# Performance work log

Hardware: AMD Instinct MI355X
Metric: run time of the kernel (lower is better)

## Reference

```python
import jax, jax.numpy as jnp
import numpy as np
from jax import lax

B, L, C = 128, 200, 300          # batch, text_len, embed_channels
K = 128                          # conv_num_kernel
WS = (2, 3, 4, 5)                # conv_kernel_size
A = 5000                         # num_api
F = 64                           # feature_channels


def setup_inputs() -> dict:
    key = jax.random.key(0)
    ks = jax.random.split(key, 24)
    s = 0.02
    inp = {"x": jax.random.normal(ks[0], (B, L, C), dtype=jnp.float32)}
    for i, ws in enumerate(WS):
        inp[f"conv_w{ws}"] = jax.random.normal(ks[1 + i], (K, C, ws), dtype=jnp.float32) * s
        inp[f"conv_b{ws}"] = jnp.zeros((K,), dtype=jnp.float32)
    D = K * len(WS)
    inp["sc_fcl_w"] = jax.random.normal(ks[5], (A, D), dtype=jnp.float32) * s
    inp["sc_fcl_b"] = jnp.zeros((A,), dtype=jnp.float32)
    inp["fic_fc_w"] = jax.random.normal(ks[6], (F, D), dtype=jnp.float32) * s
    inp["fic_fc_b"] = jnp.zeros((F,), dtype=jnp.float32)
    inp["emb"] = jax.random.uniform(ks[7], (F, A), dtype=jnp.float32)  # torch.rand
    inp["mlp_w1"] = jax.random.normal(ks[8], (F, 2 * F), dtype=jnp.float32) * s
    inp["mlp_b1"] = jnp.zeros((F,), dtype=jnp.float32)
    inp["mlp_w2"] = jax.random.normal(ks[9], (1, F), dtype=jnp.float32) * s
    inp["mlp_b2"] = jnp.zeros((1,), dtype=jnp.float32)
    inp["fic_fcl_w"] = jax.random.normal(ks[10], (A, 2 * A), dtype=jnp.float32) * s
    inp["fic_fcl_b"] = jnp.zeros((A,), dtype=jnp.float32)
    inp["fusion_w"] = jax.random.normal(ks[11], (A, 2 * A), dtype=jnp.float32) * s
    inp["fusion_b"] = jnp.zeros((A,), dtype=jnp.float32)
    inp["task_w"] = jax.random.normal(ks[12], (A, A), dtype=jnp.float32) * s
    inp["task_b"] = jnp.zeros((A,), dtype=jnp.float32)
    return inp


def _textcnn(x_t, conv_ws, conv_bs):
    # x_t: (B, C, L); each branch: conv1d VALID -> relu -> global max over width -> (B, K)
    feats = []
    for w, b in zip(conv_ws, conv_bs):
        y = lax.conv_general_dilated(x_t, w, (1,), 'VALID',
                                     dimension_numbers=('NCH', 'OIH', 'NCH'))
        y = jax.nn.relu(y + b[None, :, None])
        feats.append(jnp.max(y, axis=2))  # full-width max-pool -> (B, K)
    # torch: cat along width dim=2 of (B,K,1) then view(B,-1) -> kernel-window index fastest
    return jnp.stack(feats, axis=2).reshape(x_t.shape[0], -1)  # (B, K*len(WS))


def reference(x, conv_w2, conv_b2, conv_w3, conv_b3, conv_w4, conv_b4,
              conv_w5, conv_b5, sc_fcl_w, sc_fcl_b, fic_fc_w, fic_fc_b, emb,
              mlp_w1, mlp_b1, mlp_w2, mlp_b2, fic_fcl_w, fic_fcl_b,
              fusion_w, fusion_b, task_w, task_b):
    x_t = jnp.transpose(x, (0, 2, 1))  # (B, C, L)
    e = _textcnn(x_t, (conv_w2, conv_w3, conv_w4, conv_w5),
                 (conv_b2, conv_b3, conv_b4, conv_b5))  # (B, D)

    u_sc = e @ sc_fcl_w.T + sc_fcl_b          # (B, A)
    u_sc_trans = e @ fic_fc_w.T + fic_fc_b    # (B, F)
    u_mm = u_sc_trans @ emb                   # (B, A)

    # Batched form of the per-sample repeat/concat + MLP loop:
    # concat(u_rep, emb.T) @ W1.T  ==  u @ W1[:, :F].T (bcast over A) + emb.T @ W1[:, F:].T
    h = (u_sc_trans @ mlp_w1[:, :F].T)[:, None, :] \
        + (emb.T @ mlp_w1[:, F:].T)[None, :, :] + mlp_b1  # (B, A, F)
    u_mlp = jnp.tanh(jnp.einsum('baf,f->ba', h, mlp_w2[0]) + mlp_b2[0])  # (B, A)

    u_fic = jnp.tanh(jnp.concatenate([u_mm, u_mlp], axis=1) @ fic_fcl_w.T + fic_fcl_b)
    u_mmf = jnp.concatenate([u_sc, u_fic], axis=1) @ fusion_w.T + fusion_b
    task = u_mmf @ task_w.T + task_b          # (B, A)
    return task
```

## Files before the change

### kernel.cpp

```cpp
#include <hip/hip_runtime.h>
#include <math.h>

#define B_ 128
#define L_ 200
#define C_ 300
#define K_ 128
#define A_ 5000
#define F_ 64
#define D_ 512
#define CP_ 320
#define LP_ 260
#define NPAD_ 5056
#define KP2_ 10048
#define KP1_ 5056

typedef __attribute__((ext_vector_type(8))) short bf16x8;
typedef __attribute__((ext_vector_type(8))) short short8;
typedef __attribute__((ext_vector_type(4))) float f32x4;

#define MFMA(a,b,c) __builtin_amdgcn_mfma_f32_16x16x32_bf16(a,b,c,0,0,0)

static __device__ __forceinline__ unsigned short f2bf(float f) {
    unsigned u = __float_as_uint(f);
    unsigned r = (u + 0x7FFFu + ((u >> 16) & 1u)) >> 16;
    return (unsigned short)r;
}

#define OFF_XP     ((size_t)0)
#define OFF_PART   ((size_t)0)
#define OFF_WP     ((size_t)5324800)
#define OFF_E      ((size_t)5611520)
#define OFF_EBF    ((size_t)5677056)
#define OFF_UMBF   ((size_t)5324800)
#define OFF_UMMFBF ((size_t)5324800)
#define OFF_UST    ((size_t)5967872)
#define OFF_VB     ((size_t)5976064)
#define OFF_S2     ((size_t)5976128)
#define OFF_T      ((size_t)5976256)
#define OFF_UFBF   ((size_t)5981312)

__global__ __launch_bounds__(320) void prep_x_kernel(const float* __restrict__ x, short* __restrict__ xp)
{
    const int row = blockIdx.x;
    const int b   = blockIdx.y;
    const int c   = threadIdx.x;
    float v = 0.f;
    if (row < L_ && c < C_) v = x[((size_t)b * L_ + row) * C_ + c];
    xp[((size_t)b * LP_ + row) * CP_ + c] = (short)f2bf(v);
}

__global__ void prep_w_kernel(const float* __restrict__ w2, const float* __restrict__ w3,
                              const float* __restrict__ w4, const float* __restrict__ w5,
                              short* __restrict__ wp)
{
    const int idx = blockIdx.x * 256 + threadIdx.x;
    if (idx >= 128 * 14 * CP_) return;
    int off, wsz; const float* src;
    if (idx < 81920)       { off = idx;          wsz = 2; src = w2; }
    else if (idx < 204800) { off = idx - 81920;  wsz = 3; src = w3; }
    else if (idx < 368640) { off = idx - 204800; wsz = 4; src = w4; }
    else                   { off = idx - 368640; wsz = 5; src = w5; }
    const int k   = off / (wsz * CP_);
    const int r   = off % (wsz * CP_);
    const int tap = r / CP_;
    const int c   = r % CP_;
    float v = 0.f;
    if (c < C_) v = src[((size_t)k * C_ + c) * wsz + tap];
    wp[idx] = (short)f2bf(v);
}

__global__ __launch_bounds__(512) void conv_gemm2_kernel(
    const short* __restrict__ xp, const short* __restrict__ wp,
    const float* __restrict__ b2, const float* __restrict__ b3,
    const float* __restrict__ b4, const float* __restrict__ b5,
    float* __restrict__ e)
{
    const int b  = blockIdx.x;
    const int br = blockIdx.y;
    const int nt = blockIdx.z;
    const int wsz  = br + 2;
    const int Pout = 199 - br;
    const int wbase = (br == 0) ? 0 : (br == 1) ? 81920 : (br == 2) ? 204800 : 368640;

    const int tid  = threadIdx.x;
    const int wave = tid >> 6;
    const int lane = tid & 63;
    const int mw   = wave & 3;
    const int nw   = wave >> 2;

    __shared__ short lA[260 * 36];
    __shared__ short lB[5 * 64 * 36];
    __shared__ float smax[4][64];

    f32x4 acc[4][2];
    #pragma unroll
    for (int mf = 0; mf < 4; ++mf)
        #pragma unroll
        for (int nf = 0; nf < 2; ++nf)
            acc[mf][nf] = (f32x4){0.f, 0.f, 0.f, 0.f};

    for (int cc = 0; cc < 10; ++cc) {
        for (int ch = tid; ch < 1040; ch += 512) {
            const int row = ch >> 2, half = ch & 3;
            *(short8*)(lA + row * 36 + half * 8) =
                *(const short8*)(xp + ((size_t)b * LP_ + row) * CP_ + cc * 32 + half * 8);
        }
        for (int ch = tid; ch < wsz * 256; ch += 512) {
            const int tap = ch >> 8;
            const int r2  = ch & 255;
            const int fil = r2 >> 2, half = r2 & 3;
            *(short8*)(lB + (tap * 64 + fil) * 36 + half * 8) =
                *(const short8*)(wp + wbase + (size_t)(nt * 64 + fil) * (wsz * CP_) + tap * CP_ + cc * 32 + half * 8);
        }
        __syncthreads();
        for (int tap = 0; tap < wsz; ++tap) {
            bf16x8 af[4], bfr[2];
            #pragma unroll
            for (int mf = 0; mf < 4; ++mf)
                af[mf] = *(const bf16x8*)(lA + (mw * 64 + mf * 16 + (lane & 15) + tap) * 36 + (lane >> 4) * 8);
            #pragma unroll
            for (int nf = 0; nf < 2; ++nf)
                bfr[nf] = *(const bf16x8*)(lB + (tap * 64 + nw * 32 + nf * 16 + (lane & 15)) * 36 + (lane >> 4) * 8);
            #pragma unroll
            for (int mf = 0; mf < 4; ++mf)
                #pragma unroll
                for (int nf = 0; nf < 2; ++nf)
                    acc[mf][nf] = MFMA(af[mf], bfr[nf], acc[mf][nf]);
        }
        __syncthreads();
    }

    float vm0 = -1e30f, vm1 = -1e30f;
    #pragma unroll
    for (int mf = 0; mf < 4; ++mf) {
        const int rowbase = mw * 64 + mf * 16 + (lane >> 4) * 4;
        #pragma unroll
        for (int r = 0; r < 4; ++r) {
            const bool valid = (rowbase + r) < Pout;
            vm0 = fmaxf(vm0, valid ? acc[mf][0][r] : -1e30f);
            vm1 = fmaxf(vm1, valid ? acc[mf][1][r] : -1e30f);
        }
    }
    vm0 = fmaxf(vm0, __shfl_xor(vm0, 16)); vm0 = fmaxf(vm0, __shfl_xor(vm0, 32));
    vm1 = fmaxf(vm1, __shfl_xor(vm1, 16)); vm1 = fmaxf(vm1, __shfl_xor(vm1, 32));
    if (lane < 16) {
        smax[mw][nw * 32 + lane]      = vm0;
        smax[mw][nw * 32 + 16 + lane] = vm1;
    }
    __syncthreads();
    if (tid < 64) {
        const float m = fmaxf(fmaxf(smax[0][tid], smax[1][tid]), fmaxf(smax[2][tid], smax[3][tid]));
        const int k = nt * 64 + tid;
        const float* bp = (br == 0) ? b2 : (br == 1) ? b3 : (br == 2) ? b4 : b5;
        e[(size_t)b * D_ + k * 4 + br] = fmaxf(bp[k] + m, 0.f);
    }
}

__global__ void prep_u_kernel(const float* __restrict__ src, int srcld,
                              short* __restrict__ dst, int ncols, int Kpad)
{
    const int idx = blockIdx.x * 256 + threadIdx.x;
    if (idx >= B_ * Kpad) return;
    const int b = idx / Kpad;
    const int c = idx % Kpad;
    float v = (c < ncols) ? src[(size_t)b * srcld + c] : 0.f;
    dst[idx] = (short)f2bf(v);
}

__global__ __launch_bounds__(512) void gemm2_kernel(
    const short* __restrict__ Abf, int Kpad,
    const float* __restrict__ W, int K, int N,
    int steps_per_z, float* __restrict__ partial)
{
    const int n0 = blockIdx.x * 64;
    const int total = Kpad >> 6;
    const int sbeg = blockIdx.y * steps_per_z;
    const int send = min(sbeg + steps_per_z, total);

    const int tid  = threadIdx.x;
    const int wave = tid >> 6;
    const int lane = tid & 63;
    const int mw   = wave & 3;
    const int nw   = wave >> 2;

    __shared__ short lA[128 * 68];
    __shared__ short lB[64 * 68];

    const int arow = tid >> 2, ac0 = (tid & 3) * 16;
    const int fil  = tid >> 3, wc0 = (tid & 7) * 8;

    f32x4 acc[2][2];
    #pragma unroll
    for (int mf = 0; mf < 2; ++mf)
        #pragma unroll
        for (int nf = 0; nf < 2; ++nf)
            acc[mf][nf] = (f32x4){0.f, 0.f, 0.f, 0.f};

    short8 ra0, ra1;
    float4 rw0, rw1;
    const bool wrow_ok = (n0 + fil) < N;

    {
        const int kb = sbeg * 64;
        ra0 = *(const short8*)(Abf + (size_t)arow * Kpad + kb + ac0);
        ra1 = *(const short8*)(Abf + (size_t)arow * Kpad + kb + ac0 + 8);
        rw0 = make_float4(0.f,0.f,0.f,0.f); rw1 = rw0;
        if (wrow_ok && (kb + wc0) < K)     rw0 = *(const float4*)(W + (size_t)(n0 + fil) * K + kb + wc0);
        if (wrow_ok && (kb + wc0 + 4) < K) rw1 = *(const float4*)(W + (size_t)(n0 + fil) * K + kb + wc0 + 4);
    }

    for (int s = sbeg; s < send; ++s) {
        __syncthreads();
        *(short8*)(lA + arow * 68 + ac0)     = ra0;
        *(short8*)(lA + arow * 68 + ac0 + 8) = ra1;
        {
            short8 wb;
            wb[0]=(short)f2bf(rw0.x); wb[1]=(short)f2bf(rw0.y); wb[2]=(short)f2bf(rw0.z); wb[3]=(short)f2bf(rw0.w);
            wb[4]=(short)f2bf(rw1.x); wb[5]=(short)f2bf(rw1.y); wb[6]=(short)f2bf(rw1.z); wb[7]=(short)f2bf(rw1.w);
            *(short8*)(lB + fil * 68 + wc0) = wb;
        }
        if (s + 1 < send) {
            const int kb = (s + 1) * 64;
            ra0 = *(const short8*)(Abf + (size_t)arow * Kpad + kb + ac0);
            ra1 = *(const short8*)(Abf + (size_t)arow * Kpad + kb + ac0 + 8);
            float4 t0 = make_float4(0.f,0.f,0.f,0.f), t1 = t0;
            if (wrow_ok && (kb + wc0) < K)     t0 = *(const float4*)(W + (size_t)(n0 + fil) * K + kb + wc0);
            if (wrow_ok && (kb + wc0 + 4) < K) t1 = *(const float4*)(W + (size_t)(n0 + fil) * K + kb + wc0 + 4);
            rw0 = t0; rw1 = t1;
        }
        __syncthreads();
        #pragma unroll
        for (int ks = 0; ks < 2; ++ks) {
            bf16x8 af[2], bfr[2];
            #pragma unroll
            for (int mf = 0; mf < 2; ++mf)
                af[mf] = *(const bf16x8*)(lA + (mw * 32 + mf * 16 + (lane & 15)) * 68 + ks * 32 + (lane >> 4) * 8);
            #pragma unroll
            for (int nf = 0; nf < 2; ++nf)
                bfr[nf] = *(const bf16x8*)(lB + (nw * 32 + nf * 16 + (lane & 15)) * 68 + ks * 32 + (lane >> 4) * 8);
            #pragma unroll
            for (int mf = 0; mf < 2; ++mf)
                #pragma unroll
                for (int nf = 0; nf < 2; ++nf)
                    acc[mf][nf] = MFMA(af[mf], bfr[nf], acc[mf][nf]);
        }
    }

    #pragma unroll
    for (int mf = 0; mf < 2; ++mf)
        #pragma unroll
        for (int nf = 0; nf < 2; ++nf)
            #pragma unroll
            for (int r = 0; r < 4; ++r) {
                const int row = mw * 32 + mf * 16 + (lane >> 4) * 4 + r;
                const int col = nw * 32 + nf * 16 + (lane & 15);
                partial[((size_t)blockIdx.y * B_ + row) * NPAD_ + n0 + col] = acc[mf][nf][r];
            }
}

__global__ void reduce2_kernel(const float* __restrict__ partial, const float* __restrict__ bias,
                               float* __restrict__ outf, short* __restrict__ outb,
                               int N, int ldo, int ooff, int js, int act)
{
    const int idx = blockIdx.x * 256 + threadIdx.x;
    if (idx >= B_ * N) return;
    const int n = idx % N;
    const int b = idx / N;
    float s = bias[n];
    for (int k = 0; k < js; ++k) s += partial[((size_t)k * B_ + b) * NPAD_ + n];
    if (act) s = tanhf(s);
    if (outb) outb[(size_t)b * ldo + ooff + n] = (short)f2bf(s);
    else      outf[(size_t)b * ldo + ooff + n] = s;
}

__global__ __launch_bounds__(256) void ust_kernel(
    const float* __restrict__ e, const float* __restrict__ W,
    const float* __restrict__ bias, float* __restrict__ ust)
{
    const int b = blockIdx.x;
    const int f = threadIdx.x >> 2;
    const int q = threadIdx.x & 3;
    const float* er = e + (size_t)b * D_ + q * 128;
    const float* wr = W + (size_t)f * D_ + q * 128;
    float acc = 0.f;
    #pragma unroll
    for (int j = 0; j < 128; j += 4) {
        const float4 ev = *(const float4*)(er + j);
        const float4 wv = *(const float4*)(wr + j);
        acc += ev.x*wv.x + ev.y*wv.y + ev.z*wv.z + ev.w*wv.w;
    }
    acc += __shfl_xor(acc, 1);
    acc += __shfl_xor(acc, 2);
    if (q == 0) ust[(size_t)b * F_ + f] = acc + bias[f];
}

__global__ void prep_kernel(const float* __restrict__ mlp_w1, const float* __restrict__ mlp_b1,
                            const float* __restrict__ mlp_w2, const float* __restrict__ mlp_b2,
                            const float* __restrict__ ust,
                            float* __restrict__ vB, float* __restrict__ s2)
{
    __shared__ float vA[64];
    __shared__ float csh;
    const int tid = threadIdx.x;
    if (tid < 64) {
        float a = 0.f;
        for (int f = 0; f < 64; ++f) a += mlp_w2[f] * mlp_w1[f * 128 + tid];
        vA[tid] = a;
    } else {
        const int g = tid - 64;
        float bsum = 0.f;
        for (int f = 0; f < 64; ++f) bsum += mlp_w2[f] * mlp_w1[f * 128 + 64 + g];
        vB[g] = bsum;
    }
    if (tid == 0) {
        float c = mlp_b2[0];
        for (int f = 0; f < 64; ++f) c += mlp_b1[f] * mlp_w2[f];
        csh = c;
    }
    __syncthreads();
    float s = csh;
    const float* ub = ust + (size_t)tid * F_;
    for (int g = 0; g < 64; ++g) s += ub[g] * vA[g];
    s2[tid] = s;
}

__global__ void ta_kernel(const float* __restrict__ emb, const float* __restrict__ vB,
                          float* __restrict__ t)
{
    __shared__ float v[64];
    if (threadIdx.x < 64) v[threadIdx.x] = vB[threadIdx.x];
    __syncthreads();
    const int a = blockIdx.x * 256 + threadIdx.x;
    if (a < A_) {
        float acc = 0.f;
        #pragma unroll
        for (int g = 0; g < 64; ++g) acc += v[g] * emb[(size_t)g * A_ + a];
        t[a] = acc;
    }
}

__global__ void um2_kernel(const float* __restrict__ ust, const float* __restrict__ emb,
                           const float* __restrict__ s2, const float* __restrict__ t,
                           short* __restrict__ umb)
{
    const int b = blockIdx.y;
    __shared__ float us[64];
    if (threadIdx.x < 64) us[threadIdx.x] = ust[(size_t)b * F_ + threadIdx.x];
    __syncthreads();
    const int a = blockIdx.x * 256 + threadIdx.x;
    if (a < A_) {
        float acc = 0.f;
        #pragma unroll
        for (int g = 0; g < 64; ++g) acc += us[g] * emb[(size_t)g * A_ + a];
        umb[(size_t)b * KP2_ + a] = (short)f2bf(acc);
        umb[(size_t)b * KP2_ + A_ + a] = (short)f2bf(tanhf(s2[b] + t[a]));
    } else if (a < A_ + 48) {
        umb[(size_t)b * KP2_ + A_ + a] = 0;
    }
}

__global__ void pad_kernel(short* __restrict__ buf, int ld, int c0, int n)
{
    const int b = blockIdx.x;
    for (int c = threadIdx.x; c < n; c += 64)
        buf[(size_t)b * ld + c0 + c] = 0;
}

extern "C" void kernel_launch(void* const* d_in, const int* in_sizes, int n_in,
                              void* d_out, int out_size, void* d_ws, size_t ws_size,
                              hipStream_t stream)
{
    const float* x       = (const float*)d_in[0];
    const float* conv_w2 = (const float*)d_in[1];
    const float* conv_b2 = (const float*)d_in[2];
    const float* conv_w3 = (const float*)d_in[3];
    const float* conv_b3 = (const float*)d_in[4];
    const float* conv_w4 = (const float*)d_in[5];
    const float* conv_b4 = (const float*)d_in[6];
    const float* conv_w5 = (const float*)d_in[7];
    const float* conv_b5 = (const float*)d_in[8];
    const float* sc_fcl_w = (const float*)d_in[9];
    const float* sc_fcl_b = (const float*)d_in[10];
    const float* fic_fc_w = (const float*)d_in[11];
    const float* fic_fc_b = (const float*)d_in[12];
    const float* emb      = (const float*)d_in[13];
    const float* mlp_w1   = (const float*)d_in[14];
    const float* mlp_b1   = (const float*)d_in[15];
    const float* mlp_w2   = (const float*)d_in[16];
    const float* mlp_b2   = (const float*)d_in[17];
    const float* fic_fcl_w = (const float*)d_in[18];
    const float* fic_fcl_b = (const float*)d_in[19];
    const float* fusion_w  = (const float*)d_in[20];
    const float* fusion_b  = (const float*)d_in[21];
    const float* task_w    = (const float*)d_in[22];
    const float* task_b    = (const float*)d_in[23];

    float* ws = (float*)d_ws;
    short* xp     = (short*)(ws + OFF_XP);
    float* part   = ws + OFF_PART;
    short* wp     = (short*)(ws + OFF_WP);
    float* e      = ws + OFF_E;
    short* ebf    = (short*)(ws + OFF_EBF);
    short* umbf   = (short*)(ws + OFF_UMBF);
    short* ummfbf = (short*)(ws + OFF_UMMFBF);
    float* ust    = ws + OFF_UST;
    float* vB     = ws + OFF_VB;
    float* s2     = ws + OFF_S2;
    float* t      = ws + OFF_T;
    short* ufbf   = (short*)(ws + OFF_UFBF);
    float* out    = (float*)d_out;

    prep_x_kernel<<<dim3(LP_, B_), CP_, 0, stream>>>(x, xp);
    prep_w_kernel<<<(128*14*CP_ + 255)/256, 256, 0, stream>>>(conv_w2, conv_w3, conv_w4, conv_w5, wp);

    conv_gemm2_kernel<<<dim3(B_, 4, 2), 512, 0, stream>>>(xp, wp, conv_b2, conv_b3, conv_b4, conv_b5, e);

    prep_u_kernel<<<(B_*D_ + 255)/256, 256, 0, stream>>>(e, D_, ebf, D_, D_);

    gemm2_kernel<<<dim3(79, 4), 512, 0, stream>>>(ebf, D_, sc_fcl_w, D_, A_, 2, part);
    reduce2_kernel<<<(B_*A_ + 255)/256, 256, 0, stream>>>(part, sc_fcl_b, nullptr, ufbf, A_, KP2_, 0, 4, 0);
    pad_kernel<<<B_, 64, 0, stream>>>(ufbf, KP2_, 2*A_, 48);

    ust_kernel<<<B_, 256, 0, stream>>>(e, fic_fc_w, fic_fc_b, ust);

    prep_kernel<<<1, 128, 0, stream>>>(mlp_w1, mlp_b1, mlp_w2, mlp_b2, ust, vB, s2);
    ta_kernel<<<(A_ + 255)/256, 256, 0, stream>>>(emb, vB, t);
    um2_kernel<<<dim3(20, B_), 256, 0, stream>>>(ust, emb, s2, t, umbf);

    gemm2_kernel<<<dim3(79, 8), 512, 0, stream>>>(umbf, KP2_, fic_fcl_w, 2*A_, A_, 20, part);
    reduce2_kernel<<<(B_*A_ + 255)/256, 256, 0, stream>>>(part, fic_fcl_b, nullptr, ufbf, A_, KP2_, A_, 8, 1);

    gemm2_kernel<<<dim3(79, 8), 512, 0, stream>>>(ufbf, KP2_, fusion_w, 2*A_, A_, 20, part);
    reduce2_kernel<<<(B_*A_ + 255)/256, 256, 0, stream>>>(part, fusion_b, nullptr, ummfbf, A_, KP1_, 0, 8, 0);
    pad_kernel<<<B_, 64, 0, stream>>>(ummfbf, KP1_, A_, 56);

    gemm2_kernel<<<dim3(79, 8), 512, 0, stream>>>(ummfbf, KP1_, task_w, A_, A_, 10, part);
    reduce2_kernel<<<(B_*A_ + 255)/256, 256, 0, stream>>>(part, task_b, out, nullptr, A_, A_, 0, 8, 0);
}
```

Baseline: 328.3 us.

## Prefetch conv tiles, fuse bf16 conversions and padding, widen split-K

The conv kernel now prefetches the next channel chunk into registers while computing the current one, and writes the bf16 copy of its output directly, which removes the separate prep_u kernel. The ta and um kernels are merged so emb is read once for both dot products. Zero-padding moves into the reduce kernel, eliminating the pad kernels. Split-K for the large GEMMs rises from 8 to 12 slices, and the workspace is relaid out so partial sums no longer alias the activation buffers. The trade is more partial-sum traffic in the reductions and extra register pressure in the conv kernel.

```diff
diff --git a/kernel.cpp b/kernel.cpp
--- a/kernel.cpp
+++ b/kernel.cpp
@@ -13,6 +13,7 @@
 #define NPAD_ 5056
 #define KP2_ 10048
 #define KP1_ 5056
+#define ZMAX_ 12
 
 typedef __attribute__((ext_vector_type(8))) short bf16x8;
 typedef __attribute__((ext_vector_type(8))) short short8;
@@ -27,17 +28,16 @@
 }
 
 #define OFF_XP     ((size_t)0)
-#define OFF_PART   ((size_t)0)
 #define OFF_WP     ((size_t)5324800)
 #define OFF_E      ((size_t)5611520)
 #define OFF_EBF    ((size_t)5677056)
-#define OFF_UMBF   ((size_t)5324800)
-#define OFF_UMMFBF ((size_t)5324800)
-#define OFF_UST    ((size_t)5967872)
-#define OFF_VB     ((size_t)5976064)
-#define OFF_S2     ((size_t)5976128)
-#define OFF_T      ((size_t)5976256)
-#define OFF_UFBF   ((size_t)5981312)
+#define OFF_UST    ((size_t)5693440)
+#define OFF_VB     ((size_t)5701632)
+#define OFF_S2     ((size_t)5701696)
+#define OFF_UMBF   ((size_t)5701824)
+#define OFF_UFBF   ((size_t)6344896)
+#define OFF_UMMFBF ((size_t)6987968)
+#define OFF_PART   ((size_t)7311552)
 
 __global__ __launch_bounds__(320) void prep_x_kernel(const float* __restrict__ x, short* __restrict__ xp)
 {
@@ -69,11 +69,11 @@
     wp[idx] = (short)f2bf(v);
 }
 
-__global__ __launch_bounds__(512) void conv_gemm2_kernel(
+__global__ __launch_bounds__(512) void conv_gemm3_kernel(
     const short* __restrict__ xp, const short* __restrict__ wp,
     const float* __restrict__ b2, const float* __restrict__ b3,
     const float* __restrict__ b4, const float* __restrict__ b5,
-    float* __restrict__ e)
+    float* __restrict__ e, short* __restrict__ ebf)
 {
     const int b  = blockIdx.x;
     const int br = blockIdx.y;
@@ -92,6 +92,14 @@
     __shared__ short lB[5 * 64 * 36];
     __shared__ float smax[4][64];
 
+    const int nbB = wsz * 256;
+    const bool hA2 = (tid < 16);
+    const bool hB1 = (tid + 512 < nbB);
+    const bool hB2 = (tid + 1024 < nbB);
+
+    const short* xbase = xp + (size_t)b * LP_ * CP_;
+    const short* wpb   = wp + wbase + (size_t)(nt * 64) * (wsz * CP_);
+
     f32x4 acc[4][2];
     #pragma unroll
     for (int mf = 0; mf < 4; ++mf)
@@ -99,20 +107,35 @@
         for (int nf = 0; nf < 2; ++nf)
             acc[mf][nf] = (f32x4){0.f, 0.f, 0.f, 0.f};
 
+    short8 a0, a1, a2, bb0, bb1, bb2;
+
+    #define LDA(ch, cc) (*(const short8*)(xbase + (size_t)((ch) >> 2) * CP_ + (cc) * 32 + ((ch) & 3) * 8))
+    #define LDB(ch, cc) (*(const short8*)(wpb + (size_t)((((ch) & 255) >> 2)) * (wsz * CP_) + ((ch) >> 8) * CP_ + (cc) * 32 + (((ch) & 255) & 3) * 8))
+
+    a0 = LDA(tid, 0); a1 = LDA(tid + 512, 0);
+    if (hA2) a2 = LDA(tid + 1024, 0);
+    bb0 = LDB(tid, 0);
+    if (hB1) bb1 = LDB(tid + 512, 0);
+    if (hB2) bb2 = LDB(tid + 1024, 0);
+
     for (int cc = 0; cc < 10; ++cc) {
-        for (int ch = tid; ch < 1040; ch += 512) {
-            const int row = ch >> 2, half = ch & 3;
-            *(short8*)(lA + row * 36 + half * 8) =
-                *(const short8*)(xp + ((size_t)b * LP_ + row) * CP_ + cc * 32 + half * 8);
-        }
-        for (int ch = tid; ch < wsz * 256; ch += 512) {
-            const int tap = ch >> 8;
-            const int r2  = ch & 255;
-            const int fil = r2 >> 2, half = r2 & 3;
-            *(short8*)(lB + (tap * 64 + fil) * 36 + half * 8) =
-                *(const short8*)(wp + wbase + (size_t)(nt * 64 + fil) * (wsz * CP_) + tap * CP_ + cc * 32 + half * 8);
-        }
         __syncthreads();
+        {
+            int ch = tid;        *(short8*)(lA + (ch >> 2) * 36 + (ch & 3) * 8) = a0;
+            ch = tid + 512;      *(short8*)(lA + (ch >> 2) * 36 + (ch & 3) * 8) = a1;
+            if (hA2) { ch = tid + 1024; *(short8*)(lA + (ch >> 2) * 36 + (ch & 3) * 8) = a2; }
+            ch = tid;            *(short8*)(lB + (((ch >> 8) << 6) + ((ch & 255) >> 2)) * 36 + ((ch & 255) & 3) * 8) = bb0;
+            if (hB1) { ch = tid + 512;  *(short8*)(lB + (((ch >> 8) << 6) + ((ch & 255) >> 2)) * 36 + ((ch & 255) & 3) * 8) = bb1; }
+            if (hB2) { ch = tid + 1024; *(short8*)(lB + (((ch >> 8) << 6) + ((ch & 255) >> 2)) * 36 + ((ch & 255) & 3) * 8) = bb2; }
+        }
+        __syncthreads();
+        if (cc + 1 < 10) {
+            a0 = LDA(tid, cc + 1); a1 = LDA(tid + 512, cc + 1);
+            if (hA2) a2 = LDA(tid + 1024, cc + 1);
+            bb0 = LDB(tid, cc + 1);
+            if (hB1) bb1 = LDB(tid + 512, cc + 1);
+            if (hB2) bb2 = LDB(tid + 1024, cc + 1);
+        }
         for (int tap = 0; tap < wsz; ++tap) {
             bf16x8 af[4], bfr[2];
             #pragma unroll
@@ -127,8 +150,9 @@
                 for (int nf = 0; nf < 2; ++nf)
                     acc[mf][nf] = MFMA(af[mf], bfr[nf], acc[mf][nf]);
         }
-        __syncthreads();
-    }
+    }
+    #undef LDA
+    #undef LDB
 
     float vm0 = -1e30f, vm1 = -1e30f;
     #pragma unroll
@@ -152,22 +176,13 @@
         const float m = fmaxf(fmaxf(smax[0][tid], smax[1][tid]), fmaxf(smax[2][tid], smax[3][tid]));
         const int k = nt * 64 + tid;
         const float* bp = (br == 0) ? b2 : (br == 1) ? b3 : (br == 2) ? b4 : b5;
-        e[(size_t)b * D_ + k * 4 + br] = fmaxf(bp[k] + m, 0.f);
-    }
-}
-
-__global__ void prep_u_kernel(const float* __restrict__ src, int srcld,
-                              short* __restrict__ dst, int ncols, int Kpad)
-{
-    const int idx = blockIdx.x * 256 + threadIdx.x;
-    if (idx >= B_ * Kpad) return;
-    const int b = idx / Kpad;
-    const int c = idx % Kpad;
-    float v = (c < ncols) ? src[(size_t)b * srcld + c] : 0.f;
-    dst[idx] = (short)f2bf(v);
-}
-
-__global__ __launch_bounds__(512) void gemm2_kernel(
+        const float val = fmaxf(bp[k] + m, 0.f);
+        e[(size_t)b * D_ + k * 4 + br] = val;
+        ebf[(size_t)b * D_ + k * 4 + br] = (short)f2bf(val);
+    }
+}
+
+__global__ __launch_bounds__(512) void gemm3_kernel(
     const short* __restrict__ Abf, int Kpad,
     const float* __restrict__ W, int K, int N,
     int steps_per_z, float* __restrict__ partial)
@@ -219,6 +234,7 @@
             wb[4]=(short)f2bf(rw1.x); wb[5]=(short)f2bf(rw1.y); wb[6]=(short)f2bf(rw1.z); wb[7]=(short)f2bf(rw1.w);
             *(short8*)(lB + fil * 68 + wc0) = wb;
         }
+        __syncthreads();
         if (s + 1 < send) {
             const int kb = (s + 1) * 64;
             ra0 = *(const short8*)(Abf + (size_t)arow * Kpad + kb + ac0);
@@ -228,7 +244,6 @@
             if (wrow_ok && (kb + wc0 + 4) < K) t1 = *(const float4*)(W + (size_t)(n0 + fil) * K + kb + wc0 + 4);
             rw0 = t0; rw1 = t1;
         }
-        __syncthreads();
         #pragma unroll
         for (int ks = 0; ks < 2; ++ks) {
             bf16x8 af[2], bfr[2];
@@ -260,12 +275,14 @@
 
 __global__ void reduce2_kernel(const float* __restrict__ partial, const float* __restrict__ bias,
                                float* __restrict__ outf, short* __restrict__ outb,
-                               int N, int ldo, int ooff, int js, int act)
-{
+                               int N, int ldo, int ooff, int js, int act, int padn)
+{
+    const int Ntot = N + padn;
     const int idx = blockIdx.x * 256 + threadIdx.x;
-    if (idx >= B_ * N) return;
-    const int n = idx % N;
-    const int b = idx / N;
+    if (idx >= B_ * Ntot) return;
+    const int n = idx % Ntot;
+    const int b = idx / Ntot;
+    if (n >= N) { outb[(size_t)b * ldo + ooff + n] = 0; return; }
     float s = bias[n];
     for (int k = 0; k < js; ++k) s += partial[((size_t)k * B_ + b) * NPAD_ + n];
     if (act) s = tanhf(s);
@@ -324,46 +341,32 @@
     s2[tid] = s;
 }
 
-__global__ void ta_kernel(const float* __restrict__ emb, const float* __restrict__ vB,
-                          float* __restrict__ t)
-{
-    __shared__ float v[64];
-    if (threadIdx.x < 64) v[threadIdx.x] = vB[threadIdx.x];
+__global__ void um3_kernel(const float* __restrict__ ust, const float* __restrict__ emb,
+                           const float* __restrict__ s2, const float* __restrict__ vB,
+                           short* __restrict__ umb)
+{
+    const int b = blockIdx.y;
+    __shared__ float us[64];
+    __shared__ float vb[64];
+    if (threadIdx.x < 64) {
+        us[threadIdx.x] = ust[(size_t)b * F_ + threadIdx.x];
+        vb[threadIdx.x] = vB[threadIdx.x];
+    }
     __syncthreads();
     const int a = blockIdx.x * 256 + threadIdx.x;
     if (a < A_) {
-        float acc = 0.f;
-        #pragma unroll
-        for (int g = 0; g < 64; ++g) acc += v[g] * emb[(size_t)g * A_ + a];
-        t[a] = acc;
-    }
-}
-
-__global__ void um2_kernel(const float* __restrict__ ust, const float* __restrict__ emb,
-                           const float* __restrict__ s2, const float* __restrict__ t,
-                           short* __restrict__ umb)
-{
-    const int b = blockIdx.y;
-    __shared__ float us[64];
-    if (threadIdx.x < 64) us[threadIdx.x] = ust[(size_t)b * F_ + threadIdx.x];
-    __syncthreads();
-    const int a = blockIdx.x * 256 + threadIdx.x;
-    if (a < A_) {
-        float acc = 0.f;
-        #pragma unroll
-        for (int g = 0; g < 64; ++g) acc += us[g] * emb[(size_t)g * A_ + a];
-        umb[(size_t)b * KP2_ + a] = (short)f2bf(acc);
-        umb[(size_t)b * KP2_ + A_ + a] = (short)f2bf(tanhf(s2[b] + t[a]));
+        float accm = 0.f, acct = 0.f;
+        #pragma unroll
+        for (int g = 0; g < 64; ++g) {
+            const float ev = emb[(size_t)g * A_ + a];
+            accm += us[g] * ev;
+            acct += vb[g] * ev;
+        }
+        umb[(size_t)b * KP2_ + a] = (short)f2bf(accm);
+        umb[(size_t)b * KP2_ + A_ + a] = (short)f2bf(tanhf(s2[b] + acct));
     } else if (a < A_ + 48) {
         umb[(size_t)b * KP2_ + A_ + a] = 0;
     }
-}
-
-__global__ void pad_kernel(short* __restrict__ buf, int ld, int c0, int n)
-{
-    const int b = blockIdx.x;
-    for (int c = threadIdx.x; c < n; c += 64)
-        buf[(size_t)b * ld + c0 + c] = 0;
 }
 
 extern "C" void kernel_launch(void* const* d_in, const int* in_sizes, int n_in,
@@ -397,43 +400,37 @@
 
     float* ws = (float*)d_ws;
     short* xp     = (short*)(ws + OFF_XP);
-    float* part   = ws + OFF_PART;
     short* wp     = (short*)(ws + OFF_WP);
     float* e      = ws + OFF_E;
     short* ebf    = (short*)(ws + OFF_EBF);
-    short* umbf   = (short*)(ws + OFF_UMBF);
-    short* ummfbf = (short*)(ws + OFF_UMMFBF);
     float* ust    = ws + OFF_UST;
     float* vB     = ws + OFF_VB;
     float* s2     = ws + OFF_S2;
-    float* t      = ws + OFF_T;
+    short* umbf   = (short*)(ws + OFF_UMBF);
     short* ufbf   = (short*)(ws + OFF_UFBF);
+    short* ummfbf = (short*)(ws + OFF_UMMFBF);
+    float* part   = ws + OFF_PART;
     float* out    = (float*)d_out;
 
     prep_x_kernel<<<dim3(LP_, B_), CP_, 0, stream>>>(x, xp);
     prep_w_kernel<<<(128*14*CP_ + 255)/256, 256, 0, stream>>>(conv_w2, conv_w3, conv_w4, conv_w5, wp);
 
-    conv_gemm2_kernel<<<dim3(B_, 4, 2), 512, 0, stream>>>(xp, wp, conv_b2, conv_b3, conv_b4, conv_b5, e);
-
-    prep_u_kernel<<<(B_*D_ + 255)/256, 256, 0, stream>>>(e, D_, ebf, D_, D_);
-
-    gemm2_kernel<<<dim3(79, 4), 512, 0, stream>>>(ebf, D_, sc_fcl_w, D_, A_, 2, part);
-    reduce2_kernel<<<(B_*A_ + 255)/256, 256, 0, stream>>>(part, sc_fcl_b, nullptr, ufbf, A_, KP2_, 0, 4, 0);
-    pad_kernel<<<B_, 64, 0, stream>>>(ufbf, KP2_, 2*A_, 48);
+    conv_gemm3_kernel<<<dim3(B_, 4, 2), 512, 0, stream>>>(xp, wp, conv_b2, conv_b3, conv_b4, conv_b5, e, ebf);
+
+    gemm3_kernel<<<dim3(79, 4), 512, 0, stream>>>(ebf, D_, sc_fcl_w, D_, A_, 2, part);
+    reduce2_kernel<<<(B_*A_ + 255)/256, 256, 0, stream>>>(part, sc_fcl_b, nullptr, ufbf, A_, KP2_, 0, 4, 0, 0);
 
     ust_kernel<<<B_, 256, 0, stream>>>(e, fic_fc_w, fic_fc_b, ust);
 
     prep_kernel<<<1, 128, 0, stream>>>(mlp_w1, mlp_b1, mlp_w2, mlp_b2, ust, vB, s2);
-    ta_kernel<<<(A_ + 255)/256, 256, 0, stream>>>(emb, vB, t);
-    um2_kernel<<<dim3(20, B_), 256, 0, stream>>>(ust, emb, s2, t, umbf);
-
-    gemm2_kernel<<<dim3(79, 8), 512, 0, stream>>>(umbf, KP2_, fic_fcl_w, 2*A_, A_, 20, part);
-    reduce2_kernel<<<(B_*A_ + 255)/256, 256, 0, stream>>>(part, fic_fcl_b, nullptr, ufbf, A_, KP2_, A_, 8, 1);
-
-    gemm2_kernel<<<dim3(79, 8), 512, 0, stream>>>(ufbf, KP2_, fusion_w, 2*A_, A_, 20, part);
-    reduce2_kernel<<<(B_*A_ + 255)/256, 256, 0, stream>>>(part, fusion_b, nullptr, ummfbf, A_, KP1_, 0, 8, 0);
-    pad_kernel<<<B_, 64, 0, stream>>>(ummfbf, KP1_, A_, 56);
-
-    gemm2_kernel<<<dim3(79, 8), 512, 0, stream>>>(ummfbf, KP1_, task_w, A_, A_, 10, part);
-    reduce2_kernel<<<(B_*A_ + 255)/256, 256, 0, stream>>>(part, task_b, out, nullptr, A_, A_, 0, 8, 0);
-}
+    um3_kernel<<<dim3(20, B_), 256, 0, stream>>>(ust, emb, s2, vB, umbf);
+
+    gemm3_kernel<<<dim3(79, 12), 512, 0, stream>>>(umbf, KP2_, fic_fcl_w, 2*A_, A_, 14, part);
+    reduce2_kernel<<<(B_*(A_+48) + 255)/256, 256, 0, stream>>>(part, fic_fcl_b, nullptr, ufbf, A_, KP2_, A_, 12, 1, 48);
+
+    gemm3_kernel<<<dim3(79, 12), 512, 0, stream>>>(ufbf, KP2_, fusion_w, 2*A_, A_, 14, part);
+    reduce2_kernel<<<(B_*(A_+56) + 255)/256, 256, 0, stream>>>(part, fusion_b, nullptr, ummfbf, A_, KP1_, 0, 12, 0, 56);
+
+    gemm3_kernel<<<dim3(79, 12), 512, 0, stream>>>(ummfbf, KP1_, task_w, A_, A_, 7, part);
+    reduce2_kernel<<<(B_*A_ + 255)/256, 256, 0, stream>>>(part, task_b, out, nullptr, A_, A_, 0, 12, 0, 0);
+}
```

After: 315.6 us. -3.8%, faster.
